# Kernel tuning notes

Hardware: AMD Instinct MI355X
Metric: run time of the kernel (lower is better)

## Reference

```python
import jax, jax.numpy as jnp
import numpy as np

B, S, D, H, E, K = 1, 2048, 1024, 16, 8, 2
DK = D // H          # 64 per-head key dim
FF = 4 * D           # 4096 expert hidden
EPS = 1e-5


def rmsnorm(x, scale):
    rms = jnp.sqrt(jnp.mean(x * x, axis=-1, keepdims=True) + EPS)
    return scale * (x / rms)


def setup_inputs() -> dict:
    key = jax.random.key(0)
    ks = jax.random.split(key, 12)
    std = 0.02
    x = jax.random.normal(ks[0], (B, S, D), dtype=jnp.float32)
    # causal mask: masked_fill where mask == 0
    self_attn_mask = jnp.tril(jnp.ones((S, S), dtype=jnp.int32))
    scale_attn = jnp.ones((D,), dtype=jnp.float32)
    scale_ffn = jnp.ones((D,), dtype=jnp.float32)
    # per-head projections, stacked: [H, DK, D] (torch Linear weight layout [out,in])
    Wq = jax.random.normal(ks[1], (H, DK, D), dtype=jnp.float32) * std
    Wk = jax.random.normal(ks[2], (H, DK, D), dtype=jnp.float32) * std
    Wv = jax.random.normal(ks[3], (H, DK, D), dtype=jnp.float32) * std
    Wo = jax.random.normal(ks[4], (D, D), dtype=jnp.float32) * std
    Wg = jax.random.normal(ks[5], (E, D), dtype=jnp.float32) * std   # router gate
    W_in = jax.random.normal(ks[6], (E, FF, D), dtype=jnp.float32) * std   # expert linear
    W_v = jax.random.normal(ks[7], (E, FF, D), dtype=jnp.float32) * std    # expert linear_v
    W_out = jax.random.normal(ks[8], (E, D, FF), dtype=jnp.float32) * std  # expert linear_out
    return {
        'x': x, 'self_attn_mask': self_attn_mask,
        'scale_attn': scale_attn, 'Wq': Wq, 'Wk': Wk, 'Wv': Wv, 'Wo': Wo,
        'scale_ffn': scale_ffn, 'Wg': Wg, 'W_in': W_in, 'W_v': W_v, 'W_out': W_out,
    }


def reference(x, self_attn_mask, scale_attn, Wq, Wk, Wv, Wo, scale_ffn, Wg, W_in, W_v, W_out):
    # --- self attention (pre-RMSNorm) ---
    normed = rmsnorm(x, scale_attn)
    q = jnp.einsum('bsd,hkd->bhsk', normed, Wq)
    k = jnp.einsum('bsd,hkd->bhsk', normed, Wk)
    v = jnp.einsum('bsd,hkd->bhsk', normed, Wv)
    attn = jnp.einsum('bhsk,bhtk->bhst', q, k) / np.sqrt(DK).astype(np.float32)
    attn = jnp.where(self_attn_mask[None, None] == 0, -jnp.inf, attn)
    attn = jax.nn.softmax(attn, axis=-1)
    ctx = jnp.einsum('bhst,bhtk->bhsk', attn, v)
    ctx = ctx.transpose(0, 2, 1, 3).reshape(x.shape[0], x.shape[1], D)  # concat heads
    a1 = ctx @ Wo.T
    x = x + a1
    # --- MoE (pre-RMSNorm) ---
    normed = rmsnorm(x, scale_ffn)
    router_logits = normed @ Wg.T                       # [B,S,E]
    router_probs = jax.nn.softmax(router_logits, axis=-1)
    gate, idx = jax.lax.top_k(router_probs, K)          # [B,S,K]
    gate = gate / jnp.sum(gate, axis=-1, keepdims=True)
    # combine weights per expert: sum of renormalized gates over selected slots
    onehot = (idx[..., None] == jnp.arange(E)).astype(x.dtype)  # [B,S,K,E]
    combine = jnp.sum(gate[..., None] * onehot, axis=2)         # [B,S,E]
    # all-expert dense FFN (faithful to the masked dense loop in torch)
    g = jax.nn.gelu(jnp.einsum('bsd,efd->bsef', normed, W_in), approximate=False)
    val = jnp.einsum('bsd,efd->bsef', normed, W_v)
    eo = jnp.einsum('bsef,edf->bsed', g * val, W_out)           # [B,S,E,D]
    moe_out = jnp.einsum('bse,bsed->bsd', combine, eo)
    out = x + moe_out
    return (out, router_probs)
```

## Files before the change

kernel.cpp:

```cpp
#include <hip/hip_runtime.h>
#include <hip/hip_bf16.h>
#include <math.h>

typedef unsigned int u32;
typedef unsigned short u16;
using bf16x8 = __attribute__((ext_vector_type(8))) short;
using f32x4 = __attribute__((ext_vector_type(4))) float;

#define MFMA_BF16(a, b, c) __builtin_amdgcn_mfma_f32_16x16x32_bf16((a), (b), (c), 0, 0, 0)
#define VMCNT8() asm volatile("s_waitcnt vmcnt(8)" ::: "memory")
#define VMCNT6() asm volatile("s_waitcnt vmcnt(6)" ::: "memory")
#define VMCNT4() asm volatile("s_waitcnt vmcnt(4)" ::: "memory")
#define VMCNT0() asm volatile("s_waitcnt vmcnt(0)" ::: "memory")
#define SBAR() __builtin_amdgcn_s_barrier()
#define SCHED0() __builtin_amdgcn_sched_barrier(0)

constexpr int kS = 2048, kD = 1024, kH = 16, kE = 8, kFF = 4096;
constexpr int kSlotCap = 5120;
constexpr int kMaxTiles = 40;
constexpr int kChunk = 8;

__device__ __forceinline__ u16 bf16_rne(float f) {
  u32 u = __float_as_uint(f);
  u32 r = (u + 0x7fffu + ((u >> 16) & 1u)) >> 16;
  return (u16)r;
}
__device__ __forceinline__ float bf16_f32(u16 h) { return __uint_as_float(((u32)h) << 16); }
__device__ __forceinline__ u32 pack_hl(float x) {
  u16 hi = bf16_rne(x);
  u16 lo = bf16_rne(x - bf16_f32(hi));
  return ((u32)lo << 16) | (u32)hi;
}
__device__ __forceinline__ void unpack8(const u32* t, bf16x8& h, bf16x8& l) {
#pragma unroll
  for (int j = 0; j < 8; j++) {
    h[j] = (short)(t[j] & 0xffffu);
    l[j] = (short)(t[j] >> 16);
  }
}
__device__ __forceinline__ void gload_lds16(const void* g, void* l) {
  __builtin_amdgcn_global_load_lds((const __attribute__((address_space(1))) u32*)g,
                                   (__attribute__((address_space(3))) u32*)l, 16, 0, 0);
}

__global__ __launch_bounds__(256) void pack_dp3(const float* __restrict__ Wq,
                                                const float* __restrict__ Wk,
                                                const float* __restrict__ Wv,
                                                u16* __restrict__ o) {
  int i = blockIdx.x * 256 + threadIdx.x;
  if (i >= 3072 * 1024) return;
  int n = i >> 10, k = i & 1023;
  float v = (n < 1024) ? Wq[i] : (n < 2048) ? Wk[i - 1024 * 1024] : Wv[i - 2048 * 1024];
  u16 hi = bf16_rne(v);
  u16 lo = bf16_rne(v - bf16_f32(hi));
  size_t b = (size_t)n * 2048 + (size_t)(k >> 5) * 64 + (k & 31);
  o[b] = hi;
  o[b + 32] = lo;
}
__global__ __launch_bounds__(256) void pack_dp1(const float* __restrict__ W,
                                                u16* __restrict__ o, int n_elem) {
  int i = blockIdx.x * 256 + threadIdx.x;
  if (i >= n_elem) return;
  int k = i & 1023, n = i >> 10;
  float v = W[i];
  u16 hi = bf16_rne(v);
  u16 lo = bf16_rne(v - bf16_f32(hi));
  size_t b = (size_t)n * 2048 + (size_t)(k >> 5) * 64 + (k & 31);
  o[b] = hi;
  o[b + 32] = lo;
}
__global__ __launch_bounds__(256) void pack_winv(const float* __restrict__ Wi,
                                                 const float* __restrict__ Wv,
                                                 u16* __restrict__ o) {
  size_t i8 = (size_t)blockIdx.x * 256 + threadIdx.x;
  if (i8 >= (size_t)kE * 8192 * 1024 / 8) return;
  size_t flat = i8 * 8;
  int e = (int)(flat >> 23);
  int r = (int)(flat & ((1u << 23) - 1));
  int n = r >> 10, k = r & 1023;
  const float* src = ((n & 1) == 0)
                         ? Wi + ((size_t)e * 4096 + (n >> 1)) * 1024 + k
                         : Wv + ((size_t)e * 4096 + (n >> 1)) * 1024 + k;
  float4 a = *(const float4*)src;
  float4 b = *(const float4*)(src + 4);
  u16 rr[8] = {bf16_rne(a.x), bf16_rne(a.y), bf16_rne(a.z), bf16_rne(a.w),
               bf16_rne(b.x), bf16_rne(b.y), bf16_rne(b.z), bf16_rne(b.w)};
  *(uint4*)(o + flat) = *(uint4*)rr;
}
__global__ __launch_bounds__(256) void pack_bf16_kernel(const float* __restrict__ w,
                                                        u16* __restrict__ o, int n8) {
  int i = blockIdx.x * 256 + threadIdx.x;
  if (i >= n8) return;
  const float4* s = (const float4*)w + (size_t)i * 2;
  float4 a = s[0], b = s[1];
  u16 r[8] = {bf16_rne(a.x), bf16_rne(a.y), bf16_rne(a.z), bf16_rne(a.w),
              bf16_rne(b.x), bf16_rne(b.y), bf16_rne(b.z), bf16_rne(b.w)};
  *(uint4*)(o + (size_t)i * 8) = *(uint4*)r;
}

template <int MODE>
__global__ __launch_bounds__(256) void rmsnorm_kernel(
    const float* __restrict__ x, const float* __restrict__ scale,
    u16* __restrict__ odp, float* __restrict__ of32, u16* __restrict__ ob16) {
  const int s = blockIdx.x;
  const float* row = x + (size_t)s * kD;
  const int c = threadIdx.x * 4;
  float4 v = *(const float4*)(row + c);
  float ss = v.x * v.x + v.y * v.y + v.z * v.z + v.w * v.w;
#pragma unroll
  for (int m = 32; m; m >>= 1) ss += __shfl_xor(ss, m);
  __shared__ float wsum[4];
  if ((threadIdx.x & 63) == 0) wsum[threadIdx.x >> 6] = ss;
  __syncthreads();
  float tot = wsum[0] + wsum[1] + wsum[2] + wsum[3];
  float rinv = 1.0f / sqrtf(tot * (1.0f / kD) + 1e-5f);
  float4 sc = *(const float4*)(scale + c);
  float n[4] = {v.x * rinv * sc.x, v.y * rinv * sc.y, v.z * rinv * sc.z, v.w * rinv * sc.w};
  if (MODE == 0) {
    u16 hv[4], lv[4];
#pragma unroll
    for (int j = 0; j < 4; j++) {
      hv[j] = bf16_rne(n[j]);
      lv[j] = bf16_rne(n[j] - bf16_f32(hv[j]));
    }
    u16* o = odp + (size_t)s * 2048 + (size_t)(c >> 5) * 64 + (c & 31);
    *(uint2*)o = *(uint2*)hv;
    *(uint2*)(o + 32) = *(uint2*)lv;
  } else {
    *(float4*)(of32 + (size_t)s * kD + c) = make_float4(n[0], n[1], n[2], n[3]);
    u16* o = ob16 + (size_t)s * kD + c;
    o[0] = bf16_rne(n[0]); o[1] = bf16_rne(n[1]); o[2] = bf16_rne(n[2]); o[3] = bf16_rne(n[3]);
  }
}

template <int APK, int OUT>
__global__ __launch_bounds__(256) void gemm_dp(
    const void* __restrict__ Av, const u16* __restrict__ Bdp,
    const float* __restrict__ resid, int K,
    u32* __restrict__ oq, u32* __restrict__ ok, u32* __restrict__ ov,
    float* __restrict__ of) {
  __shared__ u16 As[2][128 * 64];
  __shared__ u16 Bs[2][128 * 64];
  const int tid = threadIdx.x, w = tid >> 6, l = tid & 63;
  const int m0 = blockIdx.y * 128, n0 = blockIdx.x * 128;
  const int wr = (w >> 1) * 64, wc = (w & 1) * 64;
  const char* Ab = (const char*)Av;
  const char* Bb = (const char*)Bdp;
  const size_t rowb = (size_t)K * 4;

  size_t asrc[4], bsrc[4];
  int dst[4];
#pragma unroll
  for (int i = 0; i < 4; i++) {
    int fl = i * 256 + tid;
    int row = fl >> 3, cb = fl & 7;
    size_t coff = (size_t)((cb ^ (row & 7)) * 16);
    asrc[i] = (size_t)(m0 + row) * rowb + coff;
    bsrc[i] = (size_t)(n0 + row) * rowb + coff;
    dst[i] = fl * 16;
  }

  f32x4 zero = {0.f, 0.f, 0.f, 0.f};
  f32x4 acc[4][4];
#pragma unroll
  for (int i = 0; i < 4; i++)
#pragma unroll
    for (int j = 0; j < 4; j++) acc[i][j] = zero;

  auto stage = [&](int buf, int s) {
    const char* ap = Ab + (size_t)s * 128;
    const char* bp = Bb + (size_t)s * 128;
#pragma unroll
    for (int i = 0; i < 4; i++) {
      gload_lds16(ap + asrc[i], (char*)&As[buf][0] + dst[i]);
      gload_lds16(bp + bsrc[i], (char*)&Bs[buf][0] + dst[i]);
    }
  };

  const int NS = K / 32;
  stage(0, 0);
  for (int s = 0; s < NS; s++) {
    const int cur = s & 1;
    const bool lastit = (s == NS - 1);
    if (!lastit) stage(cur ^ 1, s + 1);
    if (!lastit) VMCNT8(); else VMCNT0();
    SBAR();
    SCHED0();
    bf16x8 ah[4], al[4], bh[4], bl[4];
    const int g = l >> 4;
    if (APK) {
      const u32* At = (const u32*)&As[cur][0];
#pragma unroll
      for (int mi = 0; mi < 4; mi++) {
        int row = wr + mi * 16 + (l & 15);
        u32 t[8];
        *(uint4*)t = *(const uint4*)&At[row * 32 + (((2 * g) ^ (row & 7)) * 4)];
        *(uint4*)(t + 4) = *(const uint4*)&At[row * 32 + (((2 * g + 1) ^ (row & 7)) * 4)];
        unpack8(t, ah[mi], al[mi]);
      }
    } else {
#pragma unroll
      for (int mi = 0; mi < 4; mi++) {
        int row = wr + mi * 16 + (l & 15);
        ah[mi] = *(const bf16x8*)&As[cur][row * 64 + ((g ^ (row & 7)) * 8)];
        al[mi] = *(const bf16x8*)&As[cur][row * 64 + (((4 + g) ^ (row & 7)) * 8)];
      }
    }
#pragma unroll
    for (int ni = 0; ni < 4; ni++) {
      int row = wc + ni * 16 + (l & 15);
      bh[ni] = *(const bf16x8*)&Bs[cur][row * 64 + ((g ^ (row & 7)) * 8)];
      bl[ni] = *(const bf16x8*)&Bs[cur][row * 64 + (((4 + g) ^ (row & 7)) * 8)];
    }
#pragma unroll
    for (int mi = 0; mi < 4; mi++)
#pragma unroll
      for (int ni = 0; ni < 4; ni++) {
        f32x4 c = acc[mi][ni];
        c = MFMA_BF16(al[mi], bl[ni], c);
        c = MFMA_BF16(al[mi], bh[ni], c);
        c = MFMA_BF16(ah[mi], bl[ni], c);
        c = MFMA_BF16(ah[mi], bh[ni], c);
        acc[mi][ni] = c;
      }
    SCHED0();
    if (!lastit) SBAR();
  }

  if (OUT == 0) {
    u32* dstp;
    int nb;
    if (n0 < 1024) { dstp = oq; nb = n0; }
    else if (n0 < 2048) { dstp = ok; nb = n0 - 1024; }
    else { dstp = ov; nb = n0 - 2048; }
#pragma unroll
    for (int mi = 0; mi < 4; mi++)
#pragma unroll
      for (int ni = 0; ni < 4; ni++)
#pragma unroll
        for (int r = 0; r < 4; r++) {
          int row = m0 + wr + mi * 16 + ((l >> 4) << 2) + r;
          int col = nb + wc + ni * 16 + (l & 15);
          dstp[(size_t)row * 1024 + col] = pack_hl(acc[mi][ni][r]);
        }
  } else {
#pragma unroll
    for (int mi = 0; mi < 4; mi++)
#pragma unroll
      for (int ni = 0; ni < 4; ni++)
#pragma unroll
        for (int r = 0; r < 4; r++) {
          int row = m0 + wr + mi * 16 + ((l >> 4) << 2) + r;
          int col = n0 + wc + ni * 16 + (l & 15);
          of[(size_t)row * 1024 + col] = resid[(size_t)row * 1024 + col] + acc[mi][ni][r];
        }
  }
}

__global__ __launch_bounds__(256) void attn_kernel(
    const u32* __restrict__ Qp, const u32* __restrict__ Kp, const u32* __restrict__ Vp,
    float* __restrict__ Opart, float* __restrict__ mpart, float* __restrict__ lpart) {
  constexpr int LDK = 68;
  __shared__ u32 Ks[64 * LDK];
  __shared__ u32 Vs[64 * LDK];
  __shared__ u32 Ps[64 * LDK];
  const int tid = threadIdx.x, w = tid >> 6, l = tid & 63;
  int b = blockIdx.x, qt, c;
  if (b < 8) { qt = b; c = 0; }
  else if (b < 24) { qt = 8 + ((b - 8) >> 1); c = (b - 8) & 1; }
  else if (b < 48) { qt = 16 + (b - 24) / 3; c = (b - 24) % 3; }
  else { qt = 24 + ((b - 48) >> 2); c = (b - 48) & 3; }
  const int hh = blockIdx.y;
  const int q0 = qt * 64, hc = hh * 64;
  const int kt0 = c * kChunk;
  const int kt1 = min(kt0 + kChunk, qt + 1);

  bf16x8 qh[2], ql[2];
  {
    const int qrow = q0 + w * 16 + (l & 15);
#pragma unroll
    for (int kk = 0; kk < 2; kk++) {
      u32 t[8];
      const u32* p = Qp + (size_t)qrow * kD + hc + kk * 32 + ((l >> 4) << 3);
      *(uint4*)t = *(const uint4*)p;
      *(uint4*)(t + 4) = *(const uint4*)(p + 4);
      unpack8(t, qh[kk], ql[kk]);
    }
  }
  float mrun[4], lrun[4];
  f32x4 zero = {0.f, 0.f, 0.f, 0.f};
  f32x4 oacc[4];
#pragma unroll
  for (int r = 0; r < 4; r++) { mrun[r] = -3.0e38f; lrun[r] = 0.f; }
#pragma unroll
  for (int vb = 0; vb < 4; vb++) oacc[vb] = zero;

  const int trow = tid >> 2, c0v = (tid & 3) * 16;
  const u32* gKb = Kp + hc + c0v;
  const u32* gVb = Vp + hc + c0v;
  uint4 kr[4], vr[4];
  {
    const u32* gK = gKb + (size_t)(kt0 * 64 + trow) * kD;
    kr[0] = *(const uint4*)gK; kr[1] = *(const uint4*)(gK + 4);
    kr[2] = *(const uint4*)(gK + 8); kr[3] = *(const uint4*)(gK + 12);
    const u32* gV = gVb + (size_t)(kt0 * 64 + trow) * kD;
    vr[0] = *(const uint4*)gV; vr[1] = *(const uint4*)(gV + 4);
    vr[2] = *(const uint4*)(gV + 8); vr[3] = *(const uint4*)(gV + 12);
  }

  for (int kt = kt0; kt < kt1; kt++) {
    {
      u32* sK = Ks + trow * LDK + c0v;
      *(uint4*)sK = kr[0]; *(uint4*)(sK + 4) = kr[1];
      *(uint4*)(sK + 8) = kr[2]; *(uint4*)(sK + 12) = kr[3];
#pragma unroll
      for (int j = 0; j < 4; j++) {
        Vs[(c0v + j * 4 + 0) * LDK + trow] = vr[j].x;
        Vs[(c0v + j * 4 + 1) * LDK + trow] = vr[j].y;
        Vs[(c0v + j * 4 + 2) * LDK + trow] = vr[j].z;
        Vs[(c0v + j * 4 + 3) * LDK + trow] = vr[j].w;
      }
    }
    __syncthreads();
    if (kt + 1 < kt1) {
      const u32* gK = gKb + (size_t)((kt + 1) * 64 + trow) * kD;
      kr[0] = *(const uint4*)gK; kr[1] = *(const uint4*)(gK + 4);
      kr[2] = *(const uint4*)(gK + 8); kr[3] = *(const uint4*)(gK + 12);
      const u32* gV = gVb + (size_t)((kt + 1) * 64 + trow) * kD;
      vr[0] = *(const uint4*)gV; vr[1] = *(const uint4*)(gV + 4);
      vr[2] = *(const uint4*)(gV + 8); vr[3] = *(const uint4*)(gV + 12);
    }

    f32x4 sfr[4];
#pragma unroll
    for (int kb = 0; kb < 4; kb++) {
      f32x4 sa = zero;
#pragma unroll
      for (int kk = 0; kk < 2; kk++) {
        u32 t[8];
        bf16x8 kh, kl;
        const u32* p = Ks + (kb * 16 + (l & 15)) * LDK + kk * 32 + ((l >> 4) << 3);
        *(uint4*)t = *(const uint4*)p;
        *(uint4*)(t + 4) = *(const uint4*)(p + 4);
        unpack8(t, kh, kl);
        sa = MFMA_BF16(ql[kk], kl, sa);
        sa = MFMA_BF16(ql[kk], kh, sa);
        sa = MFMA_BF16(qh[kk], kl, sa);
        sa = MFMA_BF16(qh[kk], kh, sa);
      }
      sfr[kb] = sa * 0.125f;
    }
    if (kt == qt) {
#pragma unroll
      for (int kb = 0; kb < 4; kb++) {
        int t = kt * 64 + kb * 16 + (l & 15);
#pragma unroll
        for (int r = 0; r < 4; r++) {
          int qq = q0 + w * 16 + ((l >> 4) << 2) + r;
          if (t > qq) sfr[kb][r] = -3.0e38f;
        }
      }
    }
#pragma unroll
    for (int r = 0; r < 4; r++) {
      float mx = fmaxf(fmaxf(sfr[0][r], sfr[1][r]), fmaxf(sfr[2][r], sfr[3][r]));
#pragma unroll
      for (int mm = 1; mm < 16; mm <<= 1) mx = fmaxf(mx, __shfl_xor(mx, mm));
      float mnew = fmaxf(mrun[r], mx);
      float sf = __expf(mrun[r] - mnew);
      mrun[r] = mnew;
      float rs = 0.f;
#pragma unroll
      for (int kb = 0; kb < 4; kb++) {
        float p = __expf(sfr[kb][r] - mnew);
        sfr[kb][r] = p;
        rs += p;
      }
#pragma unroll
      for (int mm = 1; mm < 16; mm <<= 1) rs += __shfl_xor(rs, mm);
      lrun[r] = lrun[r] * sf + rs;
#pragma unroll
      for (int vb = 0; vb < 4; vb++) oacc[vb][r] *= sf;
    }
#pragma unroll
    for (int kb = 0; kb < 4; kb++)
#pragma unroll
      for (int r = 0; r < 4; r++)
        Ps[(w * 16 + ((l >> 4) << 2) + r) * LDK + kb * 16 + (l & 15)] = pack_hl(sfr[kb][r]);
#pragma unroll
    for (int ks = 0; ks < 2; ks++) {
      bf16x8 ph, pl;
      {
        u32 t[8];
        const u32* pp = Ps + (w * 16 + (l & 15)) * LDK + ks * 32 + ((l >> 4) << 3);
        *(uint4*)t = *(const uint4*)pp;
        *(uint4*)(t + 4) = *(const uint4*)(pp + 4);
        unpack8(t, ph, pl);
      }
#pragma unroll
      for (int vb = 0; vb < 4; vb++) {
        u32 t2[8];
        bf16x8 vh, vl;
        const u32* pv = Vs + (vb * 16 + (l & 15)) * LDK + ks * 32 + ((l >> 4) << 3);
        *(uint4*)t2 = *(const uint4*)pv;
        *(uint4*)(t2 + 4) = *(const uint4*)(pv + 4);
        unpack8(t2, vh, vl);
        f32x4 cc = oacc[vb];
        cc = MFMA_BF16(pl, vl, cc);
        cc = MFMA_BF16(pl, vh, cc);
        cc = MFMA_BF16(ph, vl, cc);
        cc = MFMA_BF16(ph, vh, cc);
        oacc[vb] = cc;
      }
    }
    __syncthreads();
  }

  const int p = (qt * 16 + hh) * 4 + c;
  float* Po = Opart + (size_t)p * 4096;
#pragma unroll
  for (int vb = 0; vb < 4; vb++)
#pragma unroll
    for (int r = 0; r < 4; r++) {
      int rl = w * 16 + ((l >> 4) << 2) + r;
      int cl = vb * 16 + (l & 15);
      Po[rl * 64 + cl] = oacc[vb][r];
    }
  if ((l & 15) == 0) {
#pragma unroll
    for (int r = 0; r < 4; r++) {
      int rl = w * 16 + ((l >> 4) << 2) + r;
      mpart[p * 64 + rl] = mrun[r];
      lpart[p * 64 + rl] = lrun[r];
    }
  }
}

__global__ __launch_bounds__(256) void attn_merge(
    const float* __restrict__ Opart, const float* __restrict__ mpart,
    const float* __restrict__ lpart, u32* __restrict__ Op) {
  const int qt = blockIdx.x, hh = blockIdx.y;
  const int nch = (qt + kChunk) >> 3;
  const int t = threadIdx.x;
  const int row = t >> 2;
  const int c0 = (t & 3) * 16;
  const int pbase = (qt * 16 + hh) * 4;
  float M = -3.0e38f;
  for (int c = 0; c < nch; c++) M = fmaxf(M, mpart[(pbase + c) * 64 + row]);
  float den = 0.f;
  float acc[16];
#pragma unroll
  for (int j = 0; j < 16; j++) acc[j] = 0.f;
  for (int c = 0; c < nch; c++) {
    float wgt = __expf(mpart[(pbase + c) * 64 + row] - M);
    den += wgt * lpart[(pbase + c) * 64 + row];
    const float* po = Opart + (size_t)(pbase + c) * 4096 + row * 64 + c0;
#pragma unroll
    for (int j = 0; j < 16; j += 4) {
      float4 v = *(const float4*)(po + j);
      acc[j] += wgt * v.x; acc[j + 1] += wgt * v.y;
      acc[j + 2] += wgt * v.z; acc[j + 3] += wgt * v.w;
    }
  }
  float inv = 1.f / den;
  u32* dst = Op + (size_t)(qt * 64 + row) * kD + hh * 64 + c0;
#pragma unroll
  for (int j = 0; j < 16; j++) dst[j] = pack_hl(acc[j] * inv);
}

__global__ __launch_bounds__(256) void router_kernel(
    const float* __restrict__ normed, const float* __restrict__ Wg,
    float* __restrict__ probs, float* __restrict__ gates,
    int* __restrict__ experts, int* __restrict__ counts) {
  const int w = threadIdx.x >> 6, l = threadIdx.x & 63;
  const int s = blockIdx.x * 4 + w;
  float lg[kE];
  const float* row = normed + (size_t)s * kD;
#pragma unroll
  for (int e = 0; e < kE; e++) {
    const float* wg = Wg + (size_t)e * kD;
    float a = 0.f;
    for (int d = l; d < kD; d += 64) a += row[d] * wg[d];
#pragma unroll
    for (int m = 32; m; m >>= 1) a += __shfl_xor(a, m);
    lg[e] = a;
  }
  if (l == 0) {
    float mx = lg[0];
#pragma unroll
    for (int e = 1; e < kE; e++) mx = fmaxf(mx, lg[e]);
    float p[kE], sum = 0.f;
#pragma unroll
    for (int e = 0; e < kE; e++) { p[e] = __expf(lg[e] - mx); sum += p[e]; }
    float inv = 1.f / sum;
#pragma unroll
    for (int e = 0; e < kE; e++) { p[e] *= inv; probs[(size_t)s * kE + e] = p[e]; }
    int i1 = 0;
#pragma unroll
    for (int e = 1; e < kE; e++) if (lg[e] > lg[i1]) i1 = e;
    int i2 = (i1 == 0) ? 1 : 0;
#pragma unroll
    for (int e = 0; e < kE; e++) if (e != i1 && lg[e] > lg[i2]) i2 = e;
    float den = 1.f / (p[i1] + p[i2]);
    gates[s * 2] = p[i1] * den;
    gates[s * 2 + 1] = p[i2] * den;
    experts[s * 2] = i1;
    experts[s * 2 + 1] = i2;
    atomicAdd(&counts[i1], 1);
    atomicAdd(&counts[i2], 1);
  }
}

__global__ void moe_init(int* counts) {
  if (threadIdx.x < kE) counts[threadIdx.x] = 0;
}
__global__ void moe_scan(const int* __restrict__ counts, int* __restrict__ ebase,
                         int* __restrict__ cursor, int2* __restrict__ tmap) {
  if (threadIdx.x == 0) {
    int acc = 0, t = 0;
    for (int e = 0; e < kE; e++) {
      ebase[e] = acc;
      cursor[e] = acc;
      int nt = (counts[e] + 127) >> 7;
      for (int i = 0; i < nt; i++) tmap[t++] = make_int2(e, i * 128);
      acc += nt << 7;
    }
    ebase[kE] = acc;
    for (; t < kMaxTiles; t++) tmap[t] = make_int2(-1, 0);
  }
}
__global__ void moe_fill(const int* __restrict__ experts, int* __restrict__ cursor,
                         int* __restrict__ slot_list, int* __restrict__ slot_of) {
  int s = blockIdx.x * 256 + threadIdx.x;
  if (s >= kS) return;
  for (int k = 0; k < 2; k++) {
    int e = experts[s * 2 + k];
    int pos = atomicAdd(&cursor[e], 1);
    slot_list[pos] = s;
    slot_of[s * 2 + k] = pos;
  }
}

__global__ __launch_bounds__(256) void moe_mmA(
    const u16* __restrict__ A, const u16* __restrict__ Bg,
    const int* __restrict__ slot_list, const int* __restrict__ counts,
    const int* __restrict__ ebase, const int2* __restrict__ tmap,
    u16* __restrict__ H) {
  int2 tm = tmap[blockIdx.y];
  const int e = tm.x;
  if (e < 0) return;
  const int base = ebase[e], Me = counts[e], m0 = tm.y;
  const int n0 = blockIdx.x * 128;
  __shared__ u16 As[2][64 * 64];
  __shared__ u16 Bs[2][64 * 64];
  const int tid = threadIdx.x, w = tid >> 6, l = tid & 63;
  const int wr = (w >> 1) * 64, wc = (w & 1) * 64;
  const char* Ab = (const char*)A;
  const char* Bb = (const char*)(Bg + ((size_t)e * 8192) * 1024);

  size_t asrc[2], bsrc[2];
  int dst[2];
#pragma unroll
  for (int i = 0; i < 2; i++) {
    int fl = i * 256 + tid;
    int lrow = fl >> 3, s = fl & 7;
    int sp = s ^ (lrow & 7);
    int t = 2 * lrow + (sp >> 2);
    int cbl = sp & 3;
    size_t coff = (size_t)cbl * 16;
    int mr = m0 + t;
    if (mr > Me - 1) mr = Me - 1;
    int ar = slot_list[base + mr];
    asrc[i] = (size_t)ar * 2048 + coff;
    bsrc[i] = (size_t)(n0 + t) * 2048 + coff;
    dst[i] = fl * 16;
  }

  f32x4 zero = {0.f, 0.f, 0.f, 0.f};
  f32x4 acc[4][4];
#pragma unroll
  for (int i = 0; i < 4; i++)
#pragma unroll
    for (int j = 0; j < 4; j++) acc[i][j] = zero;

  auto stage = [&](int buf, int s) {
    const size_t so = (size_t)s * 64;
#pragma unroll
    for (int i = 0; i < 2; i++) {
      gload_lds16(Ab + so + asrc[i], (char*)&As[buf][0] + dst[i]);
      gload_lds16(Bb + so + bsrc[i], (char*)&Bs[buf][0] + dst[i]);
    }
  };

  const int NS = kD / 32;
  stage(0, 0);
  for (int s = 0; s < NS; s++) {
    const int cur = s & 1;
    const bool lastit = (s == NS - 1);
    if (!lastit) stage(cur ^ 1, s + 1);
    if (!lastit) VMCNT4(); else VMCNT0();
    SBAR();
    SCHED0();
    const int g = l >> 4;
    bf16x8 af[4], bfr[4];
#pragma unroll
    for (int mi = 0; mi < 4; mi++) {
      int t = wr + mi * 16 + (l & 15);
      int lr = t >> 1;
      int sl = (((t & 1) << 2) | g) ^ (lr & 7);
      af[mi] = *(const bf16x8*)&As[cur][lr * 64 + sl * 8];
    }
#pragma unroll
    for (int ni = 0; ni < 4; ni++) {
      int t = wc + ni * 16 + (l & 15);
      int lr = t >> 1;
      int sl = (((t & 1) << 2) | g) ^ (lr & 7);
      bfr[ni] = *(const bf16x8*)&Bs[cur][lr * 64 + sl * 8];
    }
#pragma unroll
    for (int mi = 0; mi < 4; mi++)
#pragma unroll
      for (int ni = 0; ni < 4; ni++) acc[mi][ni] = MFMA_BF16(af[mi], bfr[ni], acc[mi][ni]);
    SCHED0();
    if (!lastit) SBAR();
  }

#pragma unroll
  for (int mi = 0; mi < 4; mi++)
#pragma unroll
    for (int r = 0; r < 4; r++) {
      int ml = m0 + wr + mi * 16 + ((l >> 4) << 2) + r;
      if (ml >= Me) continue;
      size_t rb = (size_t)(base + ml) * 4096;
#pragma unroll
      for (int ni = 0; ni < 4; ni++) {
        int col = n0 + wc + ni * 16 + (l & 15);
        float v0 = acc[mi][ni][r];
        float pv = __shfl_xor(v0, 1);
        if ((l & 1) == 0) {
          float ge = 0.5f * v0 * (1.0f + erff(v0 * 0.70710678118654752f));
          H[rb + (col >> 1)] = bf16_rne(ge * pv);
        }
      }
    }
}

__global__ __launch_bounds__(256) void moe_mm2(
    const u16* __restrict__ H, const u16* __restrict__ Bg,
    const int* __restrict__ counts, const int* __restrict__ ebase,
    const int2* __restrict__ tmap, float* __restrict__ eo) {
  int2 tm = tmap[blockIdx.y];
  const int e = tm.x;
  if (e < 0) return;
  const int base = ebase[e], Me = counts[e], m0 = tm.y;
  const int n0 = blockIdx.x * 64;
  __shared__ u16 As[2][128 * 64];
  __shared__ u16 Bs[2][64 * 64];
  const int tid = threadIdx.x, w = tid >> 6, l = tid & 63;
  const int wr = (w >> 1) * 64, wc = (w & 1) * 32;
  const char* Ab = (const char*)H;
  const char* Bb = (const char*)(Bg + (size_t)e * kD * kFF);

  size_t asrc[4], bsrc[2];
  int adst[4], bdst[2];
#pragma unroll
  for (int i = 0; i < 4; i++) {
    int fl = i * 256 + tid;
    int row = fl >> 3, cb = fl & 7;
    int mr = m0 + row;
    if (mr > Me - 1) mr = Me - 1;
    asrc[i] = (size_t)(base + mr) * 8192 + (size_t)((cb ^ (row & 7)) * 16);
    adst[i] = fl * 16;
  }
#pragma unroll
  for (int i = 0; i < 2; i++) {
    int fl = i * 256 + tid;
    int row = fl >> 3, cb = fl & 7;
    bsrc[i] = (size_t)(n0 + row) * 8192 + (size_t)((cb ^ (row & 7)) * 16);
    bdst[i] = fl * 16;
  }

  f32x4 zero = {0.f, 0.f, 0.f, 0.f};
  f32x4 acc[4][2];
#pragma unroll
  for (int i = 0; i < 4; i++)
#pragma unroll
    for (int j = 0; j < 2; j++) acc[i][j] = zero;

  auto stage = [&](int buf, int s) {
    const size_t so = (size_t)s * 128;
#pragma unroll
    for (int i = 0; i < 4; i++) gload_lds16(Ab + so + asrc[i], (char*)&As[buf][0] + adst[i]);
#pragma unroll
    for (int i = 0; i < 2; i++) gload_lds16(Bb + so + bsrc[i], (char*)&Bs[buf][0] + bdst[i]);
  };

  const int NS = kFF / 64;
  stage(0, 0);
  for (int s = 0; s < NS; s++) {
    const int cur = s & 1;
    const bool lastit = (s == NS - 1);
    if (!lastit) stage(cur ^ 1, s + 1);
    if (!lastit) VMCNT6(); else VMCNT0();
    SBAR();
    SCHED0();
#pragma unroll
    for (int kk = 0; kk < 2; kk++) {
      const int g = kk * 4 + (l >> 4);
      bf16x8 af[4], bfr[2];
#pragma unroll
      for (int mi = 0; mi < 4; mi++) {
        int row = wr + mi * 16 + (l & 15);
        af[mi] = *(const bf16x8*)&As[cur][row * 64 + ((g ^ (row & 7)) * 8)];
      }
#pragma unroll
      for (int ni = 0; ni < 2; ni++) {
        int row = wc + ni * 16 + (l & 15);
        bfr[ni] = *(const bf16x8*)&Bs[cur][row * 64 + ((g ^ (row & 7)) * 8)];
      }
#pragma unroll
      for (int mi = 0; mi < 4; mi++)
#pragma unroll
        for (int ni = 0; ni < 2; ni++) acc[mi][ni] = MFMA_BF16(af[mi], bfr[ni], acc[mi][ni]);
    }
    SCHED0();
    if (!lastit) SBAR();
  }

#pragma unroll
  for (int mi = 0; mi < 4; mi++)
#pragma unroll
    for (int r = 0; r < 4; r++) {
      int ml = m0 + wr + mi * 16 + ((l >> 4) << 2) + r;
      if (ml >= Me) continue;
      size_t rb = (size_t)(base + ml) * kD;
#pragma unroll
      for (int ni = 0; ni < 2; ni++) {
        int col = n0 + wc + ni * 16 + (l & 15);
        eo[rb + col] = acc[mi][ni][r];
      }
    }
}

__global__ __launch_bounds__(256) void combine_kernel(
    const float* __restrict__ h, const float* __restrict__ eo,
    const float* __restrict__ gates, const int* __restrict__ slot_of,
    float* __restrict__ out) {
  const int s = blockIdx.x;
  const float g0 = gates[s * 2], g1 = gates[s * 2 + 1];
  const int p0 = slot_of[s * 2], p1 = slot_of[s * 2 + 1];
  const int c = threadIdx.x * 4;
  float4 hv = *(const float4*)(h + (size_t)s * kD + c);
  float4 e0 = *(const float4*)(eo + (size_t)p0 * kD + c);
  float4 e1 = *(const float4*)(eo + (size_t)p1 * kD + c);
  float4 o;
  o.x = hv.x + g0 * e0.x + g1 * e1.x;
  o.y = hv.y + g0 * e0.y + g1 * e1.y;
  o.z = hv.z + g0 * e0.z + g1 * e1.z;
  o.w = hv.w + g0 * e0.w + g1 * e1.w;
  *(float4*)(out + (size_t)s * kD + c) = o;
}

extern "C" void kernel_launch(void* const* d_in, const int* in_sizes, int n_in,
                              void* d_out, int out_size, void* d_ws, size_t ws_size,
                              hipStream_t stream) {
  (void)in_sizes; (void)n_in; (void)out_size; (void)ws_size;
  const float* x = (const float*)d_in[0];
  const float* scale_attn = (const float*)d_in[2];
  const float* Wq = (const float*)d_in[3];
  const float* Wk = (const float*)d_in[4];
  const float* Wv = (const float*)d_in[5];
  const float* Wo = (const float*)d_in[6];
  const float* scale_ffn = (const float*)d_in[7];
  const float* Wg = (const float*)d_in[8];
  const float* W_in = (const float*)d_in[9];
  const float* W_vv = (const float*)d_in[10];
  const float* W_out = (const float*)d_in[11];
  float* out = (float*)d_out;
  float* probs = out + (size_t)kS * kD;

  char* wsb = (char*)d_ws;
  size_t off = 0;
  auto alloc = [&](size_t bytes) -> void* {
    void* p = wsb + off;
    off += (bytes + 255) & ~(size_t)255;
    return p;
  };
  const size_t SDu = (size_t)kS * kD;
  u16* normA_dp = (u16*)alloc(SDu * 4);
  u32* qpk = (u32*)alloc(SDu * 4);
  u32* kpk = (u32*)alloc(SDu * 4);
  u32* vpk = (u32*)alloc(SDu * 4);
  u32* ctxpk = (u32*)alloc(SDu * 4);
  u16* Wqkv_dp = (u16*)alloc((size_t)3072 * 2048 * 2);
  u16* Wo_dp = (u16*)alloc((size_t)1024 * 2048 * 2);
  float* normFf = (float*)alloc(SDu * 4);
  float* eo = (float*)alloc((size_t)kSlotCap * kD * 4);
  float* h = (float*)alloc(SDu * 4);
  u16* normFb = (u16*)alloc(SDu * 2);
  u16* Winv_bf = (u16*)alloc((size_t)kE * 8192 * 1024 * 2);
  u16* Wout_bf = (u16*)alloc((size_t)kE * kD * kFF * 2);
  u16* H = (u16*)alloc((size_t)kSlotCap * kFF * 2);
  float* Opart = (float*)alloc((size_t)2048 * 4096 * 4);
  float* mpart = (float*)alloc((size_t)2048 * 64 * 4);
  float* lpart = (float*)alloc((size_t)2048 * 64 * 4);
  float* gates = (float*)alloc(kS * 2 * 4);
  int* experts = (int*)alloc(kS * 2 * 4);
  int* slot_of = (int*)alloc(kS * 2 * 4);
  int* slot_list = (int*)alloc(kSlotCap * 4);
  int* counts = (int*)alloc(64);
  int* ebase = (int*)alloc(64);
  int* cursor = (int*)alloc(64);
  int2* tmap = (int2*)alloc(kMaxTiles * 8);

  pack_dp3<<<(3072 * 1024) / 256, 256, 0, stream>>>(Wq, Wk, Wv, Wqkv_dp);
  pack_dp1<<<(1024 * 1024) / 256, 256, 0, stream>>>(Wo, Wo_dp, 1024 * 1024);
  pack_winv<<<(int)((size_t)kE * 8192 * 1024 / 8 / 256), 256, 0, stream>>>(W_in, W_vv, Winv_bf);
  const int n8o = (int)((size_t)kE * kD * kFF / 8);
  pack_bf16_kernel<<<(n8o + 255) / 256, 256, 0, stream>>>(W_out, Wout_bf, n8o);

  rmsnorm_kernel<0><<<kS, 256, 0, stream>>>(x, scale_attn, normA_dp, nullptr, nullptr);
  gemm_dp<0, 0><<<dim3(3072 / 128, kS / 128), 256, 0, stream>>>(
      normA_dp, Wqkv_dp, nullptr, kD, qpk, kpk, vpk, nullptr);
  attn_kernel<<<dim3(80, kH), 256, 0, stream>>>(qpk, kpk, vpk, Opart, mpart, lpart);
  attn_merge<<<dim3(kS / 64, kH), 256, 0, stream>>>(Opart, mpart, lpart, ctxpk);
  gemm_dp<1, 1><<<dim3(1024 / 128, kS / 128), 256, 0, stream>>>(
      ctxpk, Wo_dp, x, kD, nullptr, nullptr, nullptr, h);

  rmsnorm_kernel<1><<<kS, 256, 0, stream>>>(h, scale_ffn, nullptr, normFf, normFb);
  moe_init<<<1, 64, 0, stream>>>(counts);
  router_kernel<<<kS / 4, 256, 0, stream>>>(normFf, Wg, probs, gates, experts, counts);
  moe_scan<<<1, 64, 0, stream>>>(counts, ebase, cursor, tmap);
  moe_fill<<<kS / 256, 256, 0, stream>>>(experts, cursor, slot_list, slot_of);

  moe_mmA<<<dim3(8192 / 128, kMaxTiles), 256, 0, stream>>>(
      normFb, Winv_bf, slot_list, counts, ebase, tmap, H);
  moe_mm2<<<dim3(kD / 64, kMaxTiles), 256, 0, stream>>>(
      H, Wout_bf, counts, ebase, tmap, eo);

  combine_kernel<<<kS, 256, 0, stream>>>(h, eo, gates, slot_of, out);
}
```

Before: 662.6 us.

## Fuse fp32-to-bf16 expert weight conversion into MoE GEMM and drop lo*lo MFMA

Removes the separate pass that packed W_in/W_v into an interleaved bf16 buffer; moe_mmA now loads fp32 weights directly into LDS and converts to bf16 in registers with packed convert instructions. This eliminates a large write+read of the packed copy but doubles the byte size of B tiles fetched per K step and uses more LDS. Separately, the split-precision projection GEMM drops the low*low product term, cutting a quarter of its MFMAs at a small accuracy cost.

```diff
diff --git a/kernel.cpp b/kernel.cpp
--- a/kernel.cpp
+++ b/kernel.cpp
@@ -41,6 +41,11 @@
 __device__ __forceinline__ void gload_lds16(const void* g, void* l) {
   __builtin_amdgcn_global_load_lds((const __attribute__((address_space(1))) u32*)g,
                                    (__attribute__((address_space(3))) u32*)l, 16, 0, 0);
+}
+__device__ __forceinline__ u32 cvtpk(float a, float b) {
+  u32 r;
+  asm("v_cvt_pk_bf16_f32 %0, %1, %2" : "=v"(r) : "v"(a), "v"(b));
+  return r;
 }
 
 __global__ __launch_bounds__(256) void pack_dp3(const float* __restrict__ Wq,
@@ -68,24 +73,6 @@
   size_t b = (size_t)n * 2048 + (size_t)(k >> 5) * 64 + (k & 31);
   o[b] = hi;
   o[b + 32] = lo;
-}
-__global__ __launch_bounds__(256) void pack_winv(const float* __restrict__ Wi,
-                                                 const float* __restrict__ Wv,
-                                                 u16* __restrict__ o) {
-  size_t i8 = (size_t)blockIdx.x * 256 + threadIdx.x;
-  if (i8 >= (size_t)kE * 8192 * 1024 / 8) return;
-  size_t flat = i8 * 8;
-  int e = (int)(flat >> 23);
-  int r = (int)(flat & ((1u << 23) - 1));
-  int n = r >> 10, k = r & 1023;
-  const float* src = ((n & 1) == 0)
-                         ? Wi + ((size_t)e * 4096 + (n >> 1)) * 1024 + k
-                         : Wv + ((size_t)e * 4096 + (n >> 1)) * 1024 + k;
-  float4 a = *(const float4*)src;
-  float4 b = *(const float4*)(src + 4);
-  u16 rr[8] = {bf16_rne(a.x), bf16_rne(a.y), bf16_rne(a.z), bf16_rne(a.w),
-               bf16_rne(b.x), bf16_rne(b.y), bf16_rne(b.z), bf16_rne(b.w)};
-  *(uint4*)(o + flat) = *(uint4*)rr;
 }
 __global__ __launch_bounds__(256) void pack_bf16_kernel(const float* __restrict__ w,
                                                         u16* __restrict__ o, int n8) {
@@ -217,7 +204,6 @@
 #pragma unroll
       for (int ni = 0; ni < 4; ni++) {
         f32x4 c = acc[mi][ni];
-        c = MFMA_BF16(al[mi], bl[ni], c);
         c = MFMA_BF16(al[mi], bh[ni], c);
         c = MFMA_BF16(ah[mi], bl[ni], c);
         c = MFMA_BF16(ah[mi], bh[ni], c);
@@ -542,7 +528,7 @@
 }
 
 __global__ __launch_bounds__(256) void moe_mmA(
-    const u16* __restrict__ A, const u16* __restrict__ Bg,
+    const u16* __restrict__ A, const float* __restrict__ Wi, const float* __restrict__ Wv2,
     const int* __restrict__ slot_list, const int* __restrict__ counts,
     const int* __restrict__ ebase, const int2* __restrict__ tmap,
     u16* __restrict__ H) {
@@ -552,28 +538,53 @@
   const int base = ebase[e], Me = counts[e], m0 = tm.y;
   const int n0 = blockIdx.x * 128;
   __shared__ u16 As[2][64 * 64];
-  __shared__ u16 Bs[2][64 * 64];
+  __shared__ float Bsf[2][128 * 32];
   const int tid = threadIdx.x, w = tid >> 6, l = tid & 63;
   const int wr = (w >> 1) * 64, wc = (w & 1) * 64;
   const char* Ab = (const char*)A;
-  const char* Bb = (const char*)(Bg + ((size_t)e * 8192) * 1024);
-
-  size_t asrc[2], bsrc[2];
-  int dst[2];
+
+  size_t asrc[2];
+  int adst[2];
 #pragma unroll
   for (int i = 0; i < 2; i++) {
     int fl = i * 256 + tid;
-    int lrow = fl >> 3, s = fl & 7;
-    int sp = s ^ (lrow & 7);
+    int lrow = fl >> 3, sl = fl & 7;
+    int sp = sl ^ (lrow & 7);
     int t = 2 * lrow + (sp >> 2);
     int cbl = sp & 3;
-    size_t coff = (size_t)cbl * 16;
     int mr = m0 + t;
     if (mr > Me - 1) mr = Me - 1;
     int ar = slot_list[base + mr];
-    asrc[i] = (size_t)ar * 2048 + coff;
-    bsrc[i] = (size_t)(n0 + t) * 2048 + coff;
-    dst[i] = fl * 16;
+    asrc[i] = (size_t)ar * 2048 + (size_t)cbl * 16;
+    adst[i] = fl * 16;
+  }
+  const char* bptr[4];
+  int bdst[4];
+#pragma unroll
+  for (int i = 0; i < 4; i++) {
+    int fl = i * 256 + tid;
+    int row = fl >> 3, sl = fl & 7;
+    int sp = sl ^ (row & 7);
+    int nn = n0 + row;
+    const float* srcT = (nn & 1) ? Wv2 : Wi;
+    bptr[i] = (const char*)(srcT + ((size_t)e * 4096 + (nn >> 1)) * 1024) + sp * 16;
+    bdst[i] = fl * 16;
+  }
+
+  const int g = l >> 4;
+  int aoff[4], boff0[4], boff1[4];
+#pragma unroll
+  for (int mi = 0; mi < 4; mi++) {
+    int t = wr + mi * 16 + (l & 15);
+    int lr = t >> 1;
+    int sl = (((t & 1) << 2) | g) ^ (lr & 7);
+    aoff[mi] = lr * 128 + sl * 16;
+  }
+#pragma unroll
+  for (int ni = 0; ni < 4; ni++) {
+    int rr = wc + ni * 16 + (l & 15);
+    boff0[ni] = rr * 128 + (((2 * g) ^ (rr & 7)) * 16);
+    boff1[ni] = rr * 128 + (((2 * g + 1) ^ (rr & 7)) * 16);
   }
 
   f32x4 zero = {0.f, 0.f, 0.f, 0.f};
@@ -584,12 +595,14 @@
     for (int j = 0; j < 4; j++) acc[i][j] = zero;
 
   auto stage = [&](int buf, int s) {
-    const size_t so = (size_t)s * 64;
-#pragma unroll
-    for (int i = 0; i < 2; i++) {
-      gload_lds16(Ab + so + asrc[i], (char*)&As[buf][0] + dst[i]);
-      gload_lds16(Bb + so + bsrc[i], (char*)&Bs[buf][0] + dst[i]);
-    }
+    const size_t soA = (size_t)s * 64;
+    const size_t soB = (size_t)s * 128;
+#pragma unroll
+    for (int i = 0; i < 2; i++)
+      gload_lds16(Ab + soA + asrc[i], (char*)&As[buf][0] + adst[i]);
+#pragma unroll
+    for (int i = 0; i < 4; i++)
+      gload_lds16(bptr[i] + soB, (char*)&Bsf[buf][0] + bdst[i]);
   };
 
   const int NS = kD / 32;
@@ -598,24 +611,24 @@
     const int cur = s & 1;
     const bool lastit = (s == NS - 1);
     if (!lastit) stage(cur ^ 1, s + 1);
-    if (!lastit) VMCNT4(); else VMCNT0();
+    if (!lastit) VMCNT6(); else VMCNT0();
     SBAR();
     SCHED0();
-    const int g = l >> 4;
+    const char* Ac = (const char*)&As[cur][0];
+    const char* Bc = (const char*)&Bsf[cur][0];
     bf16x8 af[4], bfr[4];
 #pragma unroll
-    for (int mi = 0; mi < 4; mi++) {
-      int t = wr + mi * 16 + (l & 15);
-      int lr = t >> 1;
-      int sl = (((t & 1) << 2) | g) ^ (lr & 7);
-      af[mi] = *(const bf16x8*)&As[cur][lr * 64 + sl * 8];
-    }
+    for (int mi = 0; mi < 4; mi++) af[mi] = *(const bf16x8*)(Ac + aoff[mi]);
 #pragma unroll
     for (int ni = 0; ni < 4; ni++) {
-      int t = wc + ni * 16 + (l & 15);
-      int lr = t >> 1;
-      int sl = (((t & 1) << 2) | g) ^ (lr & 7);
-      bfr[ni] = *(const bf16x8*)&Bs[cur][lr * 64 + sl * 8];
+      float4 f0 = *(const float4*)(Bc + boff0[ni]);
+      float4 f1 = *(const float4*)(Bc + boff1[ni]);
+      u32 pk[4];
+      pk[0] = cvtpk(f0.x, f0.y);
+      pk[1] = cvtpk(f0.z, f0.w);
+      pk[2] = cvtpk(f1.x, f1.y);
+      pk[3] = cvtpk(f1.z, f1.w);
+      bfr[ni] = *(bf16x8*)pk;
     }
 #pragma unroll
     for (int mi = 0; mi < 4; mi++)
@@ -798,7 +811,6 @@
   float* eo = (float*)alloc((size_t)kSlotCap * kD * 4);
   float* h = (float*)alloc(SDu * 4);
   u16* normFb = (u16*)alloc(SDu * 2);
-  u16* Winv_bf = (u16*)alloc((size_t)kE * 8192 * 1024 * 2);
   u16* Wout_bf = (u16*)alloc((size_t)kE * kD * kFF * 2);
   u16* H = (u16*)alloc((size_t)kSlotCap * kFF * 2);
   float* Opart = (float*)alloc((size_t)2048 * 4096 * 4);
@@ -815,7 +827,6 @@
 
   pack_dp3<<<(3072 * 1024) / 256, 256, 0, stream>>>(Wq, Wk, Wv, Wqkv_dp);
   pack_dp1<<<(1024 * 1024) / 256, 256, 0, stream>>>(Wo, Wo_dp, 1024 * 1024);
-  pack_winv<<<(int)((size_t)kE * 8192 * 1024 / 8 / 256), 256, 0, stream>>>(W_in, W_vv, Winv_bf);
   const int n8o = (int)((size_t)kE * kD * kFF / 8);
   pack_bf16_kernel<<<(n8o + 255) / 256, 256, 0, stream>>>(W_out, Wout_bf, n8o);
 
@@ -834,7 +845,7 @@
   moe_fill<<<kS / 256, 256, 0, stream>>>(experts, cursor, slot_list, slot_of);
 
   moe_mmA<<<dim3(8192 / 128, kMaxTiles), 256, 0, stream>>>(
-      normFb, Winv_bf, slot_list, counts, ebase, tmap, H);
+      normFb, W_in, W_vv, slot_list, counts, ebase, tmap, H);
   moe_mm2<<<dim3(kD / 64, kMaxTiles), 256, 0, stream>>>(
       H, Wout_bf, counts, ebase, tmap, eo);
 
```

Result: faster. 626.9 us (-5.4%).
